# Kernel optimization log

Measured on AMD Instinct MI355X. Metric: run time of the kernel, lower is better.

The kernel has to match this reference:

```python
import jax, jax.numpy as jnp
import numpy as np

EMBED_DIM = 1024
NUM_HEADS = 16
SEQ = 2048
BATCH = 2


def setup_inputs() -> dict:
    key = jax.random.key(0)
    ks = jax.random.split(key, 9)
    E = EMBED_DIM
    gain = 1.0 / np.sqrt(2.0)  # xavier_uniform with gain 1/sqrt(2) (qkv_same_dim)
    limit = gain * np.sqrt(6.0 / (E + E))
    q = jax.random.normal(ks[0], (SEQ, BATCH, E), dtype=jnp.float32)
    k = jax.random.normal(ks[1], (SEQ, BATCH, E), dtype=jnp.float32)
    v = jax.random.normal(ks[2], (SEQ, BATCH, E), dtype=jnp.float32)
    Wq = jax.random.uniform(ks[3], (E, E), jnp.float32, -limit, limit)
    Wk = jax.random.uniform(ks[4], (E, E), jnp.float32, -limit, limit)
    Wv = jax.random.uniform(ks[5], (E, E), jnp.float32, -limit, limit)
    bq = jnp.zeros((E,), jnp.float32)
    bk = jnp.zeros((E,), jnp.float32)
    bv = jnp.zeros((E,), jnp.float32)
    return {"query": q, "key": k, "value": v,
            "Wq": Wq, "bq": bq, "Wk": Wk, "bk": bk, "Wv": Wv, "bv": bv}


def reference(query, key, value, Wq, bq, Wk, bk, Wv, bv):
    # Base Taylor attention path (norm_taylor=True, do_scale=True, has_out=False).
    L, B, E = query.shape
    H = NUM_HEADS
    hd = E // H
    scaling = E ** (-0.5)  # self.scaling = dim**-0.5, dim == embed_dim

    q = (query @ Wq + bq) * scaling          # (L, B, E)
    k = key @ Wk + bk                         # (S, B, E)
    v = value @ Wv + bv                       # (S, B, E)

    def split_heads(x):
        # (T, B, E) -> (B*H, T, hd)
        T = x.shape[0]
        return x.reshape(T, B * H, hd).transpose(1, 0, 2)

    qh, kh, vh = split_heads(q), split_heads(k), split_heads(v)

    # Taylor expansion of exp(qk) to first order: 1 + q.k
    attn = 1.0 + jnp.einsum('bld,bsd->bls', qh, kh)   # (B*H, L, S)
    attn = attn / attn.sum(axis=-1, keepdims=True)    # row-normalize
    out = jnp.einsum('bls,bsd->bld', attn, vh)        # (B*H, L, hd)
    out = out.transpose(1, 0, 2).reshape(L, B, E)     # (L, B, E)
    return out
```

## Files before the change

kernel.cpp:

```cpp
#include <hip/hip_runtime.h>
#include <hip/hip_bf16.h>

#define L_SEQ 2048
#define BATCH 2
#define ROWS 4096
#define E 1024
#define NH 16
#define HD 64

typedef __attribute__((ext_vector_type(4))) float f32x4;
typedef __attribute__((ext_vector_type(8))) __bf16 bf16x8;

#define SWZ(byt) ((byt) ^ ((((byt) >> 7) & 7) << 4))

__device__ __forceinline__ void gload16(const void* g, void* l) {
    __builtin_amdgcn_global_load_lds((const __attribute__((address_space(1))) void*)g,
                                     (__attribute__((address_space(3))) void*)l,
                                     16, 0, 0);
}

__global__ __launch_bounds__(256) void prep_w(const float* __restrict__ Wq,
                                              const float* __restrict__ Wk,
                                              const float* __restrict__ Wv,
                                              __bf16* __restrict__ Wt) {
    const int z = blockIdx.z;
    const float* W = (z == 0) ? Wq : ((z == 1) ? Wk : Wv);
    __bf16* dst = Wt + (size_t)z * E * E;
    __shared__ __align__(16) float t[64][65];
    const int n0 = blockIdx.x * 64, k0 = blockIdx.y * 64;
    const int r = threadIdx.x >> 2, c4 = threadIdx.x & 3;
#pragma unroll
    for (int j = 0; j < 4; ++j) {
        const float4 vv = *(const float4*)&W[(size_t)(k0 + r) * E + n0 + c4 * 16 + j * 4];
        t[r][c4 * 16 + j * 4 + 0] = vv.x;
        t[r][c4 * 16 + j * 4 + 1] = vv.y;
        t[r][c4 * 16 + j * 4 + 2] = vv.z;
        t[r][c4 * 16 + j * 4 + 3] = vv.w;
    }
    __syncthreads();
    bf16x8 o0, o1;
#pragma unroll
    for (int j = 0; j < 8; ++j) {
        o0[j] = (__bf16)t[c4 * 16 + j][r];
        o1[j] = (__bf16)t[c4 * 16 + 8 + j][r];
    }
    *(bf16x8*)&dst[(size_t)(n0 + r) * E + k0 + c4 * 16] = o0;
    *(bf16x8*)&dst[(size_t)(n0 + r) * E + k0 + c4 * 16 + 8] = o1;
}

__device__ __forceinline__ void stageB(const __bf16* __restrict__ gsrc, int row0, int kcol,
                                       char* ldsdst, int wv, int ln) {
#pragma unroll
    for (int r = 0; r < 4; ++r) {
        const int rowg = row0 + r * 32 + wv * 8 + (ln >> 3);
        const int c16 = (ln & 7) ^ (ln >> 3);
        gload16(gsrc + (size_t)rowg * E + kcol + c16 * 8,
                ldsdst + r * 4096 + wv * 1024);
    }
}

__device__ __forceinline__ void loadA_f32(const float* __restrict__ gsrc, int row0, int kcol,
                                          float4 (&o)[4][2], int wv, int ln) {
#pragma unroll
    for (int r = 0; r < 4; ++r) {
        const int rowg = row0 + r * 32 + wv * 8 + (ln >> 3);
        const int c16 = (ln & 7) ^ (ln >> 3);
        const float* p = gsrc + (size_t)rowg * E + kcol + c16 * 8;
        o[r][0] = *(const float4*)p;
        o[r][1] = *(const float4*)(p + 4);
    }
}

__device__ __forceinline__ void writeA_lds(const float4 (&a)[4][2], char* dst, int wv, int ln) {
#pragma unroll
    for (int r = 0; r < 4; ++r) {
        bf16x8 o;
        o[0] = (__bf16)a[r][0].x; o[1] = (__bf16)a[r][0].y;
        o[2] = (__bf16)a[r][0].z; o[3] = (__bf16)a[r][0].w;
        o[4] = (__bf16)a[r][1].x; o[5] = (__bf16)a[r][1].y;
        o[6] = (__bf16)a[r][1].z; o[7] = (__bf16)a[r][1].w;
        *(bf16x8*)(dst + r * 4096 + wv * 1024 + ln * 16) = o;
    }
}

__device__ __forceinline__ bf16x8 fragld(const char* base, int row, int kk, int kg) {
    return *(const bf16x8*)(base + row * 128 + ((((kk << 2) | kg) ^ (row & 7)) << 4));
}

#define PH_SYNC_BEGIN  __builtin_amdgcn_s_barrier(); \
                       asm volatile("s_waitcnt lgkmcnt(0)" ::: "memory"); \
                       __builtin_amdgcn_sched_barrier(0); \
                       __builtin_amdgcn_s_setprio(1);
#define PH_SYNC_END    __builtin_amdgcn_s_setprio(0); \
                       __builtin_amdgcn_s_barrier();

__global__ __launch_bounds__(256, 2) void gemm_qkv(const float* __restrict__ xq,
                                                   const float* __restrict__ xk,
                                                   const float* __restrict__ xv,
                                                   const __bf16* __restrict__ Wt,
                                                   const float* __restrict__ bq,
                                                   const float* __restrict__ bk,
                                                   const float* __restrict__ bv,
                                                   __bf16* __restrict__ Cb) {
    extern __shared__ __align__(16) char smem[];
    const int z = blockIdx.z;
    const float* A = (z == 0) ? xq : ((z == 1) ? xk : xv);
    const __bf16* B = Wt + (size_t)z * E * E;
    __bf16* C = Cb + (size_t)z * ROWS * E;
    const float* bias = (z == 0) ? bq : ((z == 1) ? bk : bv);
    const float alpha = (z == 0) ? 0.03125f : 1.0f;
    const int m0 = blockIdx.x * 128, n0 = blockIdx.y * 128;
    const int tid = threadIdx.x, ln = tid & 63, wv = tid >> 6;
    const int lr = ln & 15, kg = ln >> 4;
    const int wm = (wv & 1) * 64, wn = (wv >> 1) * 64;

    float4 aregA[4][2], aregB[4][2];

    stageB(B, n0, 0,  smem + 32768, wv, ln);
    stageB(B, n0, 64, smem + 49152, wv, ln);
    loadA_f32(A, m0, 0,  aregA, wv, ln);
    loadA_f32(A, m0, 64, aregB, wv, ln);
    asm volatile("s_waitcnt vmcnt(0)" ::: "memory");
    writeA_lds(aregA, smem,        wv, ln);
    writeA_lds(aregB, smem + 16384, wv, ln);
    loadA_f32(A, m0, 128, aregA, wv, ln);
    asm volatile("s_waitcnt lgkmcnt(0)" ::: "memory");
    __builtin_amdgcn_s_barrier();

    f32x4 acc[4][4] = {};
    bf16x8 Af[4][2], Bf[2][2];

#define LOAD_B(nb) \
    _Pragma("unroll") for (int nn = 0; nn < 2; ++nn) \
    _Pragma("unroll") for (int kk = 0; kk < 2; ++kk) \
        Bf[nn][kk] = fragld(cB, wn + ((nb) + nn) * 16 + lr, kk, kg);
#define QUAD(q) \
    _Pragma("unroll") for (int m = 0; m < 4; ++m) \
    _Pragma("unroll") for (int nn = 0; nn < 2; ++nn) \
    _Pragma("unroll") for (int kk = 0; kk < 2; ++kk) \
        acc[m][2 * (q) + nn] = __builtin_amdgcn_mfma_f32_16x16x32_bf16(Af[m][kk], Bf[nn][kk], acc[m][2 * (q) + nn], 0, 0, 0);

#define GBODY(TT, ALOAD, AWRITE)                                                  \
    {                                                                             \
        const int Tv = (TT);                                                      \
        const char* cA = smem + (Tv & 1) * 16384;                                 \
        const char* cB = smem + 32768 + (Tv % 3) * 16384;                         \
        char* nA = smem + (Tv & 1) * 16384;                                       \
        char* nB = smem + 32768 + ((Tv + 2) % 3) * 16384;                         \
                                                           \
        if (Tv <= 12) loadA_f32(A, m0, (Tv + 3) * 64, ALOAD, wv, ln);             \
        if (Tv <= 13) stageB(B, n0, (Tv + 2) * 64, nB, wv, ln);                   \
        _Pragma("unroll") for (int m = 0; m < 4; ++m)                             \
        _Pragma("unroll") for (int kk = 0; kk < 2; ++kk)                          \
            Af[m][kk] = fragld(cA, wm + m * 16 + lr, kk, kg);                     \
        LOAD_B(0);                                                                \
        PH_SYNC_BEGIN; QUAD(0); PH_SYNC_END;                                      \
                                                           \
        if (Tv <= 12)      { asm volatile("s_waitcnt vmcnt(12)" ::: "memory"); }  \
        else if (Tv == 13) { asm volatile("s_waitcnt vmcnt(4)"  ::: "memory"); }  \
        else if (Tv == 14) { asm volatile("s_waitcnt vmcnt(0)"  ::: "memory"); }  \
        if (Tv <= 13) writeA_lds(AWRITE, nA, wv, ln);                             \
        LOAD_B(2);                                                                \
        PH_SYNC_BEGIN; QUAD(1); PH_SYNC_END;                                      \
    }

    for (int t = 0; t < 8; ++t) {
        GBODY(2 * t,     aregB, aregA);
        GBODY(2 * t + 1, aregA, aregB);
    }
#undef GBODY
#undef LOAD_B
#undef QUAD

#pragma unroll
    for (int m = 0; m < 4; ++m) {
        const int rbase = m0 + wm + m * 16 + kg * 4;
#pragma unroll
        for (int n = 0; n < 4; ++n) {
            const int col = n0 + wn + n * 16 + lr;
            const float bcol = bias[col];
#pragma unroll
            for (int rr = 0; rr < 4; ++rr)
                C[(size_t)(rbase + rr) * E + col] = (__bf16)((acc[m][n][rr] + bcol) * alpha);
        }
    }
}

__global__ __launch_bounds__(256) void reduce_kv(const __bf16* __restrict__ Kb,
                                                 const __bf16* __restrict__ Vb,
                                                 float* __restrict__ Mpart,
                                                 float* __restrict__ ksumP,
                                                 float* __restrict__ vsumP) {
    const int bh = blockIdx.x, b = bh >> 4, h = bh & 15;
    const int ts = blockIdx.y;
    const int t0 = ts * 128;
    __shared__ __align__(16) __bf16 sK[128 * 64];
    __shared__ __align__(16) __bf16 sV[128 * 64];
    __shared__ float red_k[4][64];
    __shared__ float red_v[4][64];
    const int tid = threadIdx.x;
    const int lane = tid & 63, wave = tid >> 6;
    const int lr = lane & 15, kg = lane >> 4;

    float vk[8] = {}, vv[8] = {};
    const int d0 = (tid & 7) * 8;
#pragma unroll
    for (int i = 0; i < 4; ++i) {
        const int t = i * 32 + (tid >> 3);
        const size_t g = (size_t)((t0 + t) * 2 + b) * E + h * 64 + d0;
        const bf16x8 kv = *(const bf16x8*)&Kb[g];
        const bf16x8 vvv = *(const bf16x8*)&Vb[g];
        const int lo = (t * 128 + d0 * 2) ^ (wave << 5);
        *(bf16x8*)((char*)sK + lo) = kv;
        *(bf16x8*)((char*)sV + lo) = vvv;
#pragma unroll
        for (int j = 0; j < 8; ++j) { vk[j] += (float)kv[j]; vv[j] += (float)vvv[j]; }
    }
#pragma unroll
    for (int m = 8; m <= 32; m <<= 1)
#pragma unroll
        for (int j = 0; j < 8; ++j) {
            vk[j] += __shfl_xor(vk[j], m, 64);
            vv[j] += __shfl_xor(vv[j], m, 64);
        }
    if (lane < 8)
#pragma unroll
        for (int j = 0; j < 8; ++j) {
            red_k[wave][lane * 8 + j] = vk[j];
            red_v[wave][lane * 8 + j] = vv[j];
        }
    __syncthreads();

    f32x4 acc[4] = {};
#pragma unroll
    for (int kt = 0; kt < 4; ++kt) {
        const int tb = kt * 32;
        bf16x8 afr, bfr[4];
        const char* pv = (const char*)sV + (((tb + kg * 8) * 128 + (wave * 16 + lr) * 2) ^ (kg << 5));
#pragma unroll
        for (int j = 0; j < 8; ++j) afr[j] = *(const __bf16*)(pv + j * 128);
#pragma unroll
        for (int ni = 0; ni < 4; ++ni) {
            const char* pk = (const char*)sK + (((tb + kg * 8) * 128 + (ni * 16 + lr) * 2) ^ (kg << 5));
#pragma unroll
            for (int j = 0; j < 8; ++j) bfr[ni][j] = *(const __bf16*)(pk + j * 128);
        }
#pragma unroll
        for (int ni = 0; ni < 4; ++ni)
            acc[ni] = __builtin_amdgcn_mfma_f32_16x16x32_bf16(afr, bfr[ni], acc[ni], 0, 0, 0);
    }

    float* Mp = Mpart + ((size_t)bh * 16 + ts) * 4096;
#pragma unroll
    for (int ni = 0; ni < 4; ++ni)
#pragma unroll
        for (int rr = 0; rr < 4; ++rr)
            Mp[(wave * 16 + kg * 4 + rr) * 64 + ni * 16 + lr] = acc[ni][rr];
    if (tid < 64)
        ksumP[(bh * 16 + ts) * 64 + tid] = red_k[0][tid] + red_k[1][tid] + red_k[2][tid] + red_k[3][tid];
    else if (tid < 128) {
        const int d = tid - 64;
        vsumP[(bh * 16 + ts) * 64 + d] = red_v[0][d] + red_v[1][d] + red_v[2][d] + red_v[3][d];
    }
}

__global__ __launch_bounds__(256) void combine_m(const float* __restrict__ Mpart,
                                                 const float* __restrict__ ksumP,
                                                 const float* __restrict__ vsumP,
                                                 float* __restrict__ Mt,
                                                 float* __restrict__ ksum,
                                                 float* __restrict__ vsum) {
    const int blk = blockIdx.x, tid = threadIdx.x;
    if (blk < 256) {
        const int e2 = (blk * 256 + tid) * 2;
        const int bh = e2 >> 12, r = e2 & 4095;
        const float* src = Mpart + (size_t)bh * 16 * 4096 + r;
        float s0 = 0.f, s1 = 0.f;
#pragma unroll
        for (int ts = 0; ts < 16; ++ts) {
            s0 += src[ts * 4096];
            s1 += src[ts * 4096 + 1];
        }
        Mt[(size_t)bh * 4096 + r] = s0;
        Mt[(size_t)bh * 4096 + r + 1] = s1;
    } else if (blk < 264) {
        const int idx = (blk - 256) * 256 + tid;
        const int bh = idx >> 6, d = idx & 63;
        float s = 0.f;
#pragma unroll
        for (int ts = 0; ts < 16; ++ts) s += ksumP[bh * 1024 + ts * 64 + d];
        ksum[idx] = s;
    } else {
        const int idx = (blk - 264) * 256 + tid;
        const int bh = idx >> 6, d = idx & 63;
        float s = 0.f;
#pragma unroll
        for (int ts = 0; ts < 16; ++ts) s += vsumP[bh * 1024 + ts * 64 + d];
        vsum[idx] = s;
    }
}

__global__ __launch_bounds__(256) void taylor_out(const __bf16* __restrict__ Qb,
                                                  const float* __restrict__ Mt,
                                                  const float* __restrict__ ksum,
                                                  const float* __restrict__ vsum,
                                                  float* __restrict__ out) {
    const int b = blockIdx.y;
    const int lblk = blockIdx.x * 16;
    const int tid = threadIdx.x, lane = tid & 63, wave = tid >> 6;
    const int lr = lane & 15, kg = lane >> 4;
    __shared__ __align__(16) __bf16 sM[4][4096];
    for (int hh = 0; hh < 4; ++hh) {
        __syncthreads();
#pragma unroll
        for (int i = 0; i < 8; ++i) {
            const int idx = i * 256 + tid;
            const int hseg = idx >> 9, rem = idx & 511;
            const float* src = &Mt[(size_t)(b * 16 + hseg * 4 + hh) * 4096 + rem * 8];
            const float4 mA = *(const float4*)src;
            const float4 mB = *(const float4*)(src + 4);
            bf16x8 o;
            o[0] = (__bf16)mA.x; o[1] = (__bf16)mA.y; o[2] = (__bf16)mA.z; o[3] = (__bf16)mA.w;
            o[4] = (__bf16)mB.x; o[5] = (__bf16)mB.y; o[6] = (__bf16)mB.z; o[7] = (__bf16)mB.w;
            *(bf16x8*)((char*)&sM[hseg][0] + SWZ(rem * 16)) = o;
        }
        __syncthreads();
        const int h = wave * 4 + hh;
        const int bh = b * 16 + h;
        const int rA = (lblk + lr) * 2 + b;
        const bf16x8 a0 = *(const bf16x8*)&Qb[(size_t)rA * E + h * 64 + kg * 8];
        const bf16x8 a1 = *(const bf16x8*)&Qb[(size_t)rA * E + h * 64 + 32 + kg * 8];
        float p = 0.f;
        const float* ks = &ksum[bh * 64];
#pragma unroll
        for (int j = 0; j < 8; ++j)
            p += (float)a0[j] * ks[kg * 8 + j] + (float)a1[j] * ks[32 + kg * 8 + j];
        p += __shfl_xor(p, 16, 64);
        p += __shfl_xor(p, 32, 64);
        const float Z = 2048.0f + p;
        f32x4 acc[4] = {};
#pragma unroll
        for (int ni = 0; ni < 4; ++ni) {
            const int byt0 = (ni * 16 + lr) * 128 + kg * 16;
            const bf16x8 b0 = *(const bf16x8*)((const char*)&sM[wave][0] + SWZ(byt0));
            const bf16x8 b1 = *(const bf16x8*)((const char*)&sM[wave][0] + SWZ(byt0 + 64));
            acc[ni] = __builtin_amdgcn_mfma_f32_16x16x32_bf16(a0, b0, acc[ni], 0, 0, 0);
            acc[ni] = __builtin_amdgcn_mfma_f32_16x16x32_bf16(a1, b1, acc[ni], 0, 0, 0);
        }
        float invZ[4];
#pragma unroll
        for (int rr = 0; rr < 4; ++rr) invZ[rr] = 1.0f / __shfl(Z, kg * 4 + rr, 64);
        const float* vs = &vsum[bh * 64];
#pragma unroll
        for (int ni = 0; ni < 4; ++ni)
#pragma unroll
            for (int rr = 0; rr < 4; ++rr) {
                const int l_out = lblk + kg * 4 + rr;
                out[(size_t)(l_out * 2 + b) * E + h * 64 + ni * 16 + lr] =
                    (vs[ni * 16 + lr] + acc[ni][rr]) * invZ[rr];
            }
    }
}

extern "C" void kernel_launch(void* const* d_in, const int* in_sizes, int n_in,
                              void* d_out, int out_size, void* d_ws, size_t ws_size,
                              hipStream_t stream) {
    const float* q  = (const float*)d_in[0];
    const float* k  = (const float*)d_in[1];
    const float* v  = (const float*)d_in[2];
    const float* Wq = (const float*)d_in[3];
    const float* bq = (const float*)d_in[4];
    const float* Wk = (const float*)d_in[5];
    const float* bk = (const float*)d_in[6];
    const float* Wv = (const float*)d_in[7];
    const float* bv = (const float*)d_in[8];
    float* out = (float*)d_out;
    char* w = (char*)d_ws;
    __bf16* Wt = (__bf16*)(w);
    __bf16* Cb = (__bf16*)(w + 6291456);
    float* Mt    = (float*)(w + 31457280);
    float* ksum  = (float*)(w + 31981568);
    float* vsum  = (float*)(w + 31989760);
    float* Mpart = (float*)(w + 31997952);
    float* ksumP = (float*)(w + 40386560);
    float* vsumP = (float*)(w + 40517632);

    hipFuncSetAttribute((const void*)gemm_qkv,
                        hipFuncAttributeMaxDynamicSharedMemorySize, 81920);
    prep_w<<<dim3(16, 16, 3), 256, 0, stream>>>(Wq, Wk, Wv, Wt);
    gemm_qkv<<<dim3(32, 8, 3), 256, 81920, stream>>>(q, k, v, Wt, bq, bk, bv, Cb);
    reduce_kv<<<dim3(32, 16), 256, 0, stream>>>(Cb + (size_t)ROWS * E,
                                                Cb + 2 * (size_t)ROWS * E, Mpart, ksumP, vsumP);
    combine_m<<<272, 256, 0, stream>>>(Mpart, ksumP, vsumP, Mt, ksum, vsum);
    taylor_out<<<dim3(128, 2), 256, 0, stream>>>(Cb, Mt, ksum, vsum, out);
}
```

Measured before the change: 74.44 us.

## Restructure QKV GEMM to 8 waves with simpler single-barrier pipeline

Doubles the QKV projection GEMM block from 4 to 8 waves, so each wave computes a 64x32 output tile instead of 64x64. It replaces the two-phase barrier/setprio schedule with one barrier per K-step. It also changes the fp32 A loads to contiguous per-thread row chunks written into a swizzled LDS layout. The aims are more latency hiding and simpler synchronization, at the cost of a shallower A prefetch (one tile ahead with a full vmcnt(0) wait) and higher register and occupancy pressure.

```diff
diff --git a/kernel.cpp b/kernel.cpp
--- a/kernel.cpp
+++ b/kernel.cpp
@@ -51,50 +51,39 @@
 __device__ __forceinline__ void stageB(const __bf16* __restrict__ gsrc, int row0, int kcol,
                                        char* ldsdst, int wv, int ln) {
 #pragma unroll
-    for (int r = 0; r < 4; ++r) {
-        const int rowg = row0 + r * 32 + wv * 8 + (ln >> 3);
+    for (int r = 0; r < 2; ++r) {
+        const int rowg = row0 + r * 64 + wv * 8 + (ln >> 3);
         const int c16 = (ln & 7) ^ (ln >> 3);
         gload16(gsrc + (size_t)rowg * E + kcol + c16 * 8,
-                ldsdst + r * 4096 + wv * 1024);
-    }
-}
-
-__device__ __forceinline__ void loadA_f32(const float* __restrict__ gsrc, int row0, int kcol,
-                                          float4 (&o)[4][2], int wv, int ln) {
-#pragma unroll
-    for (int r = 0; r < 4; ++r) {
-        const int rowg = row0 + r * 32 + wv * 8 + (ln >> 3);
-        const int c16 = (ln & 7) ^ (ln >> 3);
-        const float* p = gsrc + (size_t)rowg * E + kcol + c16 * 8;
-        o[r][0] = *(const float4*)p;
-        o[r][1] = *(const float4*)(p + 4);
-    }
-}
-
-__device__ __forceinline__ void writeA_lds(const float4 (&a)[4][2], char* dst, int wv, int ln) {
-#pragma unroll
-    for (int r = 0; r < 4; ++r) {
-        bf16x8 o;
-        o[0] = (__bf16)a[r][0].x; o[1] = (__bf16)a[r][0].y;
-        o[2] = (__bf16)a[r][0].z; o[3] = (__bf16)a[r][0].w;
-        o[4] = (__bf16)a[r][1].x; o[5] = (__bf16)a[r][1].y;
-        o[6] = (__bf16)a[r][1].z; o[7] = (__bf16)a[r][1].w;
-        *(bf16x8*)(dst + r * 4096 + wv * 1024 + ln * 16) = o;
-    }
+                ldsdst + r * 8192 + wv * 1024);
+    }
+}
+
+__device__ __forceinline__ void loadA(const float* __restrict__ rowp, int kcol, int aj,
+                                      float4 (&o)[4]) {
+    const float* p = rowp + kcol + aj * 16;
+    o[0] = *(const float4*)p;
+    o[1] = *(const float4*)(p + 4);
+    o[2] = *(const float4*)(p + 8);
+    o[3] = *(const float4*)(p + 12);
+}
+
+__device__ __forceinline__ void writeA(const float4 (&a)[4], char* dst, int row, int aj) {
+    bf16x8 o0, o1;
+    o0[0] = (__bf16)a[0].x; o0[1] = (__bf16)a[0].y; o0[2] = (__bf16)a[0].z; o0[3] = (__bf16)a[0].w;
+    o0[4] = (__bf16)a[1].x; o0[5] = (__bf16)a[1].y; o0[6] = (__bf16)a[1].z; o0[7] = (__bf16)a[1].w;
+    o1[0] = (__bf16)a[2].x; o1[1] = (__bf16)a[2].y; o1[2] = (__bf16)a[2].z; o1[3] = (__bf16)a[2].w;
+    o1[4] = (__bf16)a[3].x; o1[5] = (__bf16)a[3].y; o1[6] = (__bf16)a[3].z; o1[7] = (__bf16)a[3].w;
+    const int s0 = (2 * aj) ^ (row & 7), s1 = (2 * aj + 1) ^ (row & 7);
+    *(bf16x8*)(dst + row * 128 + s0 * 16) = o0;
+    *(bf16x8*)(dst + row * 128 + s1 * 16) = o1;
 }
 
 __device__ __forceinline__ bf16x8 fragld(const char* base, int row, int kk, int kg) {
     return *(const bf16x8*)(base + row * 128 + ((((kk << 2) | kg) ^ (row & 7)) << 4));
 }
 
-#define PH_SYNC_BEGIN  __builtin_amdgcn_s_barrier(); \
-                       asm volatile("s_waitcnt lgkmcnt(0)" ::: "memory"); \
-                       __builtin_amdgcn_sched_barrier(0); \
-                       __builtin_amdgcn_s_setprio(1);
-#define PH_SYNC_END    __builtin_amdgcn_s_setprio(0); \
-                       __builtin_amdgcn_s_barrier();
-
-__global__ __launch_bounds__(256, 2) void gemm_qkv(const float* __restrict__ xq,
+__global__ __launch_bounds__(512, 4) void gemm_qkv(const float* __restrict__ xq,
                                                    const float* __restrict__ xk,
                                                    const float* __restrict__ xv,
                                                    const __bf16* __restrict__ Wt,
@@ -112,71 +101,65 @@
     const int m0 = blockIdx.x * 128, n0 = blockIdx.y * 128;
     const int tid = threadIdx.x, ln = tid & 63, wv = tid >> 6;
     const int lr = ln & 15, kg = ln >> 4;
-    const int wm = (wv & 1) * 64, wn = (wv >> 1) * 64;
-
-    float4 aregA[4][2], aregB[4][2];
-
-    stageB(B, n0, 0,  smem + 32768, wv, ln);
+    const int wm = (wv & 1) * 64, wn = (wv >> 1) * 32;
+    const int arow = tid >> 2, aj = tid & 3;
+    const float* Arow = A + (size_t)(m0 + arow) * E;
+
+    float4 aregA[4], aregB[4];
+
+    stageB(B, n0, 0, smem + 32768, wv, ln);
+    loadA(Arow, 0, aj, aregA);
     stageB(B, n0, 64, smem + 49152, wv, ln);
-    loadA_f32(A, m0, 0,  aregA, wv, ln);
-    loadA_f32(A, m0, 64, aregB, wv, ln);
     asm volatile("s_waitcnt vmcnt(0)" ::: "memory");
-    writeA_lds(aregA, smem,        wv, ln);
-    writeA_lds(aregB, smem + 16384, wv, ln);
-    loadA_f32(A, m0, 128, aregA, wv, ln);
+    writeA(aregA, smem, arow, aj);
+    loadA(Arow, 64, aj, aregA);
     asm volatile("s_waitcnt lgkmcnt(0)" ::: "memory");
     __builtin_amdgcn_s_barrier();
 
-    f32x4 acc[4][4] = {};
-    bf16x8 Af[4][2], Bf[2][2];
-
-#define LOAD_B(nb) \
-    _Pragma("unroll") for (int nn = 0; nn < 2; ++nn) \
-    _Pragma("unroll") for (int kk = 0; kk < 2; ++kk) \
-        Bf[nn][kk] = fragld(cB, wn + ((nb) + nn) * 16 + lr, kk, kg);
-#define QUAD(q) \
-    _Pragma("unroll") for (int m = 0; m < 4; ++m) \
-    _Pragma("unroll") for (int nn = 0; nn < 2; ++nn) \
-    _Pragma("unroll") for (int kk = 0; kk < 2; ++kk) \
-        acc[m][2 * (q) + nn] = __builtin_amdgcn_mfma_f32_16x16x32_bf16(Af[m][kk], Bf[nn][kk], acc[m][2 * (q) + nn], 0, 0, 0);
-
-#define GBODY(TT, ALOAD, AWRITE)                                                  \
+    f32x4 acc[4][2] = {};
+
+#define GBODY(TT, AW, AL)                                                         \
     {                                                                             \
         const int Tv = (TT);                                                      \
         const char* cA = smem + (Tv & 1) * 16384;                                 \
         const char* cB = smem + 32768 + (Tv % 3) * 16384;                         \
-        char* nA = smem + (Tv & 1) * 16384;                                       \
-        char* nB = smem + 32768 + ((Tv + 2) % 3) * 16384;                         \
-                                                           \
-        if (Tv <= 12) loadA_f32(A, m0, (Tv + 3) * 64, ALOAD, wv, ln);             \
-        if (Tv <= 13) stageB(B, n0, (Tv + 2) * 64, nB, wv, ln);                   \
-        _Pragma("unroll") for (int m = 0; m < 4; ++m)                             \
-        _Pragma("unroll") for (int kk = 0; kk < 2; ++kk)                          \
-            Af[m][kk] = fragld(cA, wm + m * 16 + lr, kk, kg);                     \
-        LOAD_B(0);                                                                \
-        PH_SYNC_BEGIN; QUAD(0); PH_SYNC_END;                                      \
-                                                           \
-        if (Tv <= 12)      { asm volatile("s_waitcnt vmcnt(12)" ::: "memory"); }  \
-        else if (Tv == 13) { asm volatile("s_waitcnt vmcnt(4)"  ::: "memory"); }  \
-        else if (Tv == 14) { asm volatile("s_waitcnt vmcnt(0)"  ::: "memory"); }  \
-        if (Tv <= 13) writeA_lds(AWRITE, nA, wv, ln);                             \
-        LOAD_B(2);                                                                \
-        PH_SYNC_BEGIN; QUAD(1); PH_SYNC_END;                                      \
+        __builtin_amdgcn_s_setprio(1);                                            \
+        _Pragma("unroll") for (int kk = 0; kk < 2; ++kk) {                        \
+            bf16x8 Af[4], Bf[2];                                                  \
+            _Pragma("unroll") for (int m = 0; m < 4; ++m)                         \
+                Af[m] = fragld(cA, wm + m * 16 + lr, kk, kg);                     \
+            _Pragma("unroll") for (int n = 0; n < 2; ++n)                         \
+                Bf[n] = fragld(cB, wn + n * 16 + lr, kk, kg);                     \
+            _Pragma("unroll") for (int m = 0; m < 4; ++m)                         \
+            _Pragma("unroll") for (int n = 0; n < 2; ++n)                         \
+                acc[m][n] = __builtin_amdgcn_mfma_f32_16x16x32_bf16(              \
+                    Af[m], Bf[n], acc[m][n], 0, 0, 0);                            \
+        }                                                                         \
+        __builtin_amdgcn_s_setprio(0);                                            \
+        if (Tv < 15) {                                                            \
+            asm volatile("s_waitcnt vmcnt(0)" ::: "memory");                      \
+            writeA(AW, smem + ((Tv + 1) & 1) * 16384, arow, aj);                  \
+            if (Tv < 14) {                                                        \
+                loadA(Arow, (Tv + 2) * 64, aj, AL);                               \
+                stageB(B, n0, (Tv + 2) * 64,                                      \
+                       smem + 32768 + ((Tv + 2) % 3) * 16384, wv, ln);            \
+            }                                                                     \
+            asm volatile("s_waitcnt lgkmcnt(0)" ::: "memory");                    \
+        }                                                                         \
+        __builtin_amdgcn_s_barrier();                                             \
     }
 
     for (int t = 0; t < 8; ++t) {
-        GBODY(2 * t,     aregB, aregA);
-        GBODY(2 * t + 1, aregA, aregB);
+        GBODY(2 * t,     aregA, aregB);
+        GBODY(2 * t + 1, aregB, aregA);
     }
 #undef GBODY
-#undef LOAD_B
-#undef QUAD
 
 #pragma unroll
     for (int m = 0; m < 4; ++m) {
         const int rbase = m0 + wm + m * 16 + kg * 4;
 #pragma unroll
-        for (int n = 0; n < 4; ++n) {
+        for (int n = 0; n < 2; ++n) {
             const int col = n0 + wn + n * 16 + lr;
             const float bcol = bias[col];
 #pragma unroll
@@ -388,7 +371,7 @@
     hipFuncSetAttribute((const void*)gemm_qkv,
                         hipFuncAttributeMaxDynamicSharedMemorySize, 81920);
     prep_w<<<dim3(16, 16, 3), 256, 0, stream>>>(Wq, Wk, Wv, Wt);
-    gemm_qkv<<<dim3(32, 8, 3), 256, 81920, stream>>>(q, k, v, Wt, bq, bk, bv, Cb);
+    gemm_qkv<<<dim3(32, 8, 3), 512, 81920, stream>>>(q, k, v, Wt, bq, bk, bv, Cb);
     reduce_kv<<<dim3(32, 16), 256, 0, stream>>>(Cb + (size_t)ROWS * E,
                                                 Cb + 2 * (size_t)ROWS * E, Mpart, ksumP, vsumP);
     combine_m<<<272, 256, 0, stream>>>(Mpart, ksumP, vsumP, Mt, ksum, vsum);
```

New measurement: 74.59 us. Within noise of the previous version (+0.2%).
